# Optimization experiments

Measured on AMD Instinct MI355X. Metric: run time of the kernel, lower is better.

## Reference

```python
import jax, jax.numpy as jnp
import numpy as np

H = 256          # hidden_size
N_NODE = 50000   # item vocab
E_FULL = 500000  # full-graph edges
B = 1024         # sessions per batch
NODES_PER = 12   # session nodes per graph (contiguous, equal sections)
N = B * NODES_PER


def setup_inputs() -> dict:
    key = jax.random.key(0)
    ks = jax.random.split(key, 20)
    stdv = 1.0 / np.sqrt(H)
    u = lambda k, shape: jax.random.uniform(k, shape, jnp.float32, -stdv, stdv)
    return dict(
        x=jax.random.randint(ks[0], (N, 1), 1, N_NODE + 1, dtype=jnp.int32),  # 1-based item ids
        batch=jnp.repeat(jnp.arange(B, dtype=jnp.int32), NODES_PER),          # sorted graph ids
        edge_index=jax.random.randint(ks[1], (2, N), 0, N, dtype=jnp.int32),
        full_graph=jax.random.randint(ks[2], (2, E_FULL), 0, N_NODE, dtype=jnp.int32),
        emb=u(ks[3], (N_NODE, H)),
        ggnn_W=u(ks[4], (H, H)),
        gru_Wih=u(ks[5], (3 * H, H)),
        gru_Whh=u(ks[6], (3 * H, H)),
        gru_bih=u(ks[7], (3 * H,)),
        gru_bhh=u(ks[8], (3 * H,)),
        W1_w=u(ks[9], (H, H)), W1_b=u(ks[10], (H,)),
        W2_w=u(ks[11], (H, H)), W2_b=u(ks[12], (H,)),
        q_w=u(ks[13], (1, H)), q_b=u(ks[14], (1,)),
        W3_w=u(ks[15], (H, 2 * H)), W3_b=u(ks[16], (H,)),
    )


def _forward(x, batch, edge_index, full_graph, emb, ggnn_W, gru_Wih, gru_Whh,
             gru_bih, gru_bhh, W1_w, W1_b, W2_w, W2_b, q_w, q_b, W3_w, W3_b):
    # --- GatedGraphConv (num_layers=1) over the full item graph ---
    src, dst = full_graph[0], full_graph[1]
    m = emb @ ggnn_W                                      # [n_node, H]
    agg = jax.ops.segment_sum(m[src], dst, num_segments=N_NODE)  # sum aggregation
    # GRUCell(agg, emb)
    gi = agg @ gru_Wih.T + gru_bih                        # [n_node, 3H]
    gh = emb @ gru_Whh.T + gru_bhh
    i_r, i_z, i_n = jnp.split(gi, 3, axis=1)
    h_r, h_z, h_n = jnp.split(gh, 3, axis=1)
    r = jax.nn.sigmoid(i_r + h_r)
    z = jax.nn.sigmoid(i_z + h_z)
    n = jnp.tanh(i_n + r * h_n)
    hidden_all = (1.0 - z) * n + z * emb                  # [n_node, H]

    # gather session nodes (x is 1-based), relu
    h2 = jax.nn.relu(hidden_all[x[:, 0] - 1])             # [N, H]

    # --- Embedding2Score: segment attention readout ---
    sections = jax.ops.segment_sum(jnp.ones_like(batch), batch, num_segments=B)
    last_idx = jnp.cumsum(sections) - 1                   # last node of each session
    v_n = h2[last_idx]                                    # [B, H]
    v_n_rep = v_n[batch]                                  # [N, H]
    gate = jax.nn.sigmoid(v_n_rep @ W1_w.T + W1_b + h2 @ W2_w.T + W2_b)
    alpha = gate @ q_w.T + q_b                            # [N, 1]
    s_g = jax.ops.segment_sum(alpha * h2, batch, num_segments=B)  # [B, H]
    s_h = jnp.concatenate([v_n, s_g], axis=1) @ W3_w.T + W3_b     # [B, H]
    scores = s_h @ emb.T                                  # [B, n_node]
    return scores, h2


def reference(x, batch, edge_index, full_graph, emb, ggnn_W, gru_Wih, gru_Whh,
              gru_bih, gru_bhh, W1_w, W1_b, W2_w, W2_b, q_w, q_b, W3_w, W3_b):
    scores, h2 = _forward(x, batch, edge_index, full_graph, emb, ggnn_W,
                          gru_Wih, gru_Whh, gru_bih, gru_bhh,
                          W1_w, W1_b, W2_w, W2_b, q_w, q_b, W3_w, W3_b)
    return scores, h2, edge_index
```

## Files before the change

### kernel.cpp

```cpp
#include <hip/hip_runtime.h>
#include <hip/hip_bf16.h>
#include <stdint.h>

#define HDIM 256
#define NNODE 50000
#define EFULL 500000
#define BSESS 1024
#define NPER 12
#define NROWS 12288
#define CAP 96

typedef __attribute__((ext_vector_type(8))) short bf16x8;
typedef __attribute__((ext_vector_type(4))) float f32x4;
typedef __attribute__((ext_vector_type(4))) unsigned short u16x4;

__device__ __forceinline__ float bf2f(unsigned short v) {
  union { unsigned u; float f; } x; x.u = ((unsigned)v) << 16; return x.f;
}
__device__ __forceinline__ unsigned short f2bf(float f) {
  union { float f; unsigned u; } x; x.f = f;
  unsigned r = x.u + 0x7fff + ((x.u >> 16) & 1);
  return (unsigned short)(r >> 16);
}

__global__ void k_init_map(int* m, int* cnt) {
  int i = blockIdx.x * 256 + threadIdx.x;
  if (i < NNODE) m[i] = -1;
  if (i < NROWS) cnt[i] = 0;
}
__global__ void k_set_map(const int* __restrict__ x, int* __restrict__ m) {
  int i = blockIdx.x * 256 + threadIdx.x;
  if (i < NROWS) atomicMax(&m[x[i] - 1], i);
}

#define CV_EMB   12800000
#define CV_WT    65536
#define CV_WIH   196608
#define CV_WHH   196608
#define CV_W1    65536
#define CV_W2    65536
#define CV_W3    131072
#define CV_BIAS  2304
#define CV_TOTAL (CV_EMB + CV_WT + CV_WIH + CV_WHH + CV_W1 + CV_W2 + CV_W3 + CV_BIAS)
__global__ void k_conv(const float* __restrict__ emb, const float* __restrict__ gw,
                       const float* __restrict__ wih, const float* __restrict__ whh,
                       const float* __restrict__ w1, const float* __restrict__ w2,
                       const float* __restrict__ w3,
                       const float* __restrict__ bih, const float* __restrict__ bhh,
                       const float* __restrict__ w1b, const float* __restrict__ w2b,
                       const float* __restrict__ w3b,
                       unsigned short* __restrict__ embB, unsigned short* __restrict__ wtB,
                       unsigned short* __restrict__ wihB, unsigned short* __restrict__ whhB,
                       unsigned short* __restrict__ w1B, unsigned short* __restrict__ w2B,
                       unsigned short* __restrict__ w3B, unsigned short* __restrict__ biasB) {
  long idx = (long)blockIdx.x * 256 + threadIdx.x;
  if (idx < CV_EMB) { embB[idx] = f2bf(emb[idx]); return; }
  idx -= CV_EMB;
  if (idx < CV_WT) {
    int j = (int)(idx >> 8), k = (int)(idx & 255);
    wtB[idx] = f2bf(gw[k * 256 + j]); return;
  }
  idx -= CV_WT;
  if (idx < CV_WIH) { wihB[idx] = f2bf(wih[idx]); return; }
  idx -= CV_WIH;
  if (idx < CV_WHH) { whhB[idx] = f2bf(whh[idx]); return; }
  idx -= CV_WHH;
  if (idx < CV_W1)  { w1B[idx] = f2bf(w1[idx]); return; }
  idx -= CV_W1;
  if (idx < CV_W2)  { w2B[idx] = f2bf(w2[idx]); return; }
  idx -= CV_W2;
  if (idx < CV_W3)  { w3B[idx] = f2bf(w3[idx]); return; }
  idx -= CV_W3;
  if (idx < 768)        { biasB[idx] = f2bf(bih[idx]); return; }
  if (idx < 1536)       { biasB[idx] = f2bf(bhh[idx - 768]); return; }
  if (idx < 1792)       { biasB[idx] = f2bf(w1b[idx - 1536]); return; }
  if (idx < 2048)       { biasB[idx] = f2bf(w2b[idx - 1792]); return; }
  if (idx < CV_BIAS)    { biasB[idx] = f2bf(w3b[idx - 2048]); return; }
}

__global__ void k_bin(const int* __restrict__ fg, const int* __restrict__ map,
                      int* __restrict__ cnt, int* __restrict__ lists) {
  int e = blockIdx.x * 256 + threadIdx.x;
  if (e >= EFULL) return;
  int cid = map[fg[EFULL + e]];
  if (cid < 0) return;
  int pos = atomicAdd(&cnt[cid], 1);
  if (pos < CAP) lists[cid * CAP + pos] = fg[e];
}

__global__ __launch_bounds__(256) void k_aggsum(const int* __restrict__ cnt,
                                                const int* __restrict__ lists,
                                                const float* __restrict__ emb,
                                                unsigned short* __restrict__ Sb) {
  int i = blockIdx.x * 4 + (threadIdx.x >> 6);
  int lane = threadIdx.x & 63;
  int n = cnt[i];
  const int* lp = lists + (size_t)i * CAP;
  float sx = 0.f, sy = 0.f, sz = 0.f, sw = 0.f;
  int j = 0;
  for (; j + 4 <= n; j += 4) {
    int s0 = lp[j], s1 = lp[j + 1], s2 = lp[j + 2], s3 = lp[j + 3];
    float4 v0 = *(const float4*)(emb + (size_t)s0 * HDIM + lane * 4);
    float4 v1 = *(const float4*)(emb + (size_t)s1 * HDIM + lane * 4);
    float4 v2 = *(const float4*)(emb + (size_t)s2 * HDIM + lane * 4);
    float4 v3 = *(const float4*)(emb + (size_t)s3 * HDIM + lane * 4);
    sx += v0.x + v1.x + v2.x + v3.x;
    sy += v0.y + v1.y + v2.y + v3.y;
    sz += v0.z + v1.z + v2.z + v3.z;
    sw += v0.w + v1.w + v2.w + v3.w;
  }
  for (; j < n; j++) {
    int s0 = lp[j];
    float4 v0 = *(const float4*)(emb + (size_t)s0 * HDIM + lane * 4);
    sx += v0.x; sy += v0.y; sz += v0.z; sw += v0.w;
  }
  u16x4 o; o.x = f2bf(sx); o.y = f2bf(sy); o.z = f2bf(sz); o.w = f2bf(sw);
  *(u16x4*)(Sb + (size_t)i * HDIM + lane * 4) = o;
}

__global__ void k_gather(const int* __restrict__ x, const int* __restrict__ map,
                         const unsigned short* __restrict__ A2, const float* __restrict__ emb,
                         unsigned short* __restrict__ aggC, unsigned short* __restrict__ embC) {
  int i = blockIdx.x;
  int lane = threadIdx.x;
  int node = x[i] - 1;
  int cid = map[node];
  if (cid < 0) cid = 0;
  *(u16x4*)(aggC + (size_t)i * HDIM + lane * 4) = *(const u16x4*)(A2 + (size_t)cid * HDIM + lane * 4);
  float4 v = *(const float4*)(emb + (size_t)node * HDIM + lane * 4);
  u16x4 o; o.x = f2bf(v.x); o.y = f2bf(v.y); o.z = f2bf(v.z); o.w = f2bf(v.w);
  *(u16x4*)(embC + (size_t)i * HDIM + lane * 4) = o;
}
__global__ void k_gru(const unsigned short* __restrict__ gi, const unsigned short* __restrict__ gh,
                      const unsigned short* __restrict__ embC,
                      unsigned short* __restrict__ h2b, float* __restrict__ h2out) {
  int idx = blockIdx.x * 256 + threadIdx.x;
  size_t base = (size_t)(idx >> 8) * 768;
  int c = idx & 255;
  float ir = bf2f(gi[base + c]), iz = bf2f(gi[base + 256 + c]), inn = bf2f(gi[base + 512 + c]);
  float hr = bf2f(gh[base + c]), hz = bf2f(gh[base + 256 + c]), hn = bf2f(gh[base + 512 + c]);
  float r = 1.f / (1.f + expf(-(ir + hr)));
  float z = 1.f / (1.f + expf(-(iz + hz)));
  float n = tanhf(inn + r * hn);
  float h = fmaxf((1.f - z) * n + z * bf2f(embC[idx]), 0.f);
  h2b[idx] = f2bf(h);
  h2out[idx] = h;
}
__global__ void k_vn(const unsigned short* __restrict__ h2b, unsigned short* __restrict__ shin) {
  int idx = blockIdx.x * 256 + threadIdx.x;
  int b = idx >> 8, c = idx & 255;
  shin[(size_t)b * 512 + c] = h2b[((size_t)b * NPER + (NPER - 1)) * 256 + c];
}
__global__ void k_alpha(const unsigned short* __restrict__ t1, const unsigned short* __restrict__ t2,
                        const int* __restrict__ batch, const float* __restrict__ qw,
                        const float* __restrict__ qb, float* __restrict__ alpha) {
  int i = blockIdx.x, lane = threadIdx.x;
  int b = batch[i];
  u16x4 a = *(const u16x4*)(t1 + (size_t)b * HDIM + lane * 4);
  u16x4 c = *(const u16x4*)(t2 + (size_t)i * HDIM + lane * 4);
  float4 q = *(const float4*)(qw + lane * 4);
  float p = 0.f;
  p += q.x / (1.f + expf(-(bf2f(a.x) + bf2f(c.x))));
  p += q.y / (1.f + expf(-(bf2f(a.y) + bf2f(c.y))));
  p += q.z / (1.f + expf(-(bf2f(a.z) + bf2f(c.z))));
  p += q.w / (1.f + expf(-(bf2f(a.w) + bf2f(c.w))));
#pragma unroll
  for (int off = 32; off > 0; off >>= 1) p += __shfl_down(p, off);
  if (lane == 0) alpha[i] = p + qb[0];
}
__global__ void k_sg(const float* __restrict__ alpha, const unsigned short* __restrict__ h2b,
                     unsigned short* __restrict__ shin) {
  int b = blockIdx.x, c = threadIdx.x;
  float s = 0.f;
#pragma unroll
  for (int j = 0; j < NPER; j++)
    s += alpha[b * NPER + j] * bf2f(h2b[((size_t)b * NPER + j) * 256 + c]);
  shin[(size_t)b * 512 + 256 + c] = f2bf(s);
}
__global__ void k_edges(const int* __restrict__ e, float* __restrict__ out) {
  int i = blockIdx.x * 256 + threadIdx.x;
  if (i < 2 * NROWS) out[i] = (float)e[i];
}

template <bool OUT_BF16>
__global__ __launch_bounds__(256) void k_gemm_nt(
    const unsigned short* __restrict__ A, int lda,
    const unsigned short* __restrict__ Bm, int ldb,
    const unsigned short* __restrict__ bias,
    void* __restrict__ C, int ldc, int M, int N, int K) {
  __shared__ __align__(16) unsigned short As[128 * 32];
  __shared__ __align__(16) unsigned short Bs[128 * 32];
  const int tid = threadIdx.x;
  const int wid = tid >> 6, lane = tid & 63;
  const int quad = lane >> 4, l15 = lane & 15;
  const int m0 = blockIdx.x * 128, n0 = blockIdx.y * 128;
  const int wm = (wid & 1) * 64, wn = (wid >> 1) * 64;
  f32x4 acc[4][4] = {};
  const int lrow = tid >> 2;
  const int lcol = (tid & 3) * 8;
  const size_t ar0 = (size_t)min(m0 + lrow, M - 1) * lda + lcol;
  const size_t ar1 = (size_t)min(m0 + lrow + 64, M - 1) * lda + lcol;
  const size_t br0 = (size_t)min(n0 + lrow, N - 1) * ldb + lcol;
  const size_t br1 = (size_t)min(n0 + lrow + 64, N - 1) * ldb + lcol;
  const int ak = quad * 8;
  for (int k0 = 0; k0 < K; k0 += 32) {
    *(float4*)&As[(size_t)tid * 8]        = *(const float4*)&A[ar0 + k0];
    *(float4*)&As[2048 + (size_t)tid * 8] = *(const float4*)&A[ar1 + k0];
    *(float4*)&Bs[(size_t)tid * 8]        = *(const float4*)&Bm[br0 + k0];
    *(float4*)&Bs[2048 + (size_t)tid * 8] = *(const float4*)&Bm[br1 + k0];
    __syncthreads();
    bf16x8 af[4], bfv[4];
#pragma unroll
    for (int mi = 0; mi < 4; mi++) af[mi] = *(const bf16x8*)&As[(wm + mi * 16 + l15) * 32 + ak];
#pragma unroll
    for (int ni = 0; ni < 4; ni++) bfv[ni] = *(const bf16x8*)&Bs[(wn + ni * 16 + l15) * 32 + ak];
#pragma unroll
    for (int mi = 0; mi < 4; mi++)
#pragma unroll
      for (int ni = 0; ni < 4; ni++)
        acc[mi][ni] = __builtin_amdgcn_mfma_f32_16x16x32_bf16(af[mi], bfv[ni], acc[mi][ni], 0, 0, 0);
    __syncthreads();
  }
#pragma unroll
  for (int mi = 0; mi < 4; mi++) {
    const int gr0 = m0 + wm + mi * 16 + quad * 4;
#pragma unroll
    for (int ni = 0; ni < 4; ni++) {
      const int gc = n0 + wn + ni * 16 + l15;
      if (gc >= N) continue;
      const float bv = bias ? bf2f(bias[gc]) : 0.f;
#pragma unroll
      for (int r = 0; r < 4; r++) {
        const int gr = gr0 + r;
        if (gr < M) {
          const float v = acc[mi][ni][r] + bv;
          if (OUT_BF16) ((unsigned short*)C)[(size_t)gr * ldc + gc] = f2bf(v);
          else          ((float*)C)[(size_t)gr * ldc + gc] = v;
        }
      }
    }
  }
}

extern "C" void kernel_launch(void* const* d_in, const int* in_sizes, int n_in,
                              void* d_out, int out_size, void* d_ws, size_t ws_size,
                              hipStream_t stream) {
  const int* x     = (const int*)d_in[0];
  const int* batch = (const int*)d_in[1];
  const int* eidx  = (const int*)d_in[2];
  const int* fg    = (const int*)d_in[3];
  const float* emb   = (const float*)d_in[4];
  const float* ggnnW = (const float*)d_in[5];
  const float* Wih   = (const float*)d_in[6];
  const float* Whh   = (const float*)d_in[7];
  const float* bih   = (const float*)d_in[8];
  const float* bhh   = (const float*)d_in[9];
  const float* W1w   = (const float*)d_in[10];
  const float* W1b   = (const float*)d_in[11];
  const float* W2w   = (const float*)d_in[12];
  const float* W2b   = (const float*)d_in[13];
  const float* qw    = (const float*)d_in[14];
  const float* qb    = (const float*)d_in[15];
  const float* W3w   = (const float*)d_in[16];
  const float* W3b   = (const float*)d_in[17];

  char* w = (char*)d_ws;
  size_t off = 0;
  auto alloc = [&](size_t bytes) { char* p = w + off; off += (bytes + 511) & ~(size_t)511; return p; };
  unsigned short* giC  = (unsigned short*)alloc((size_t)NROWS * 768 * 2);
  unsigned short* Sb   = giC;
  int*            map  = (int*)alloc((size_t)NNODE * 4);
  int*            cnt  = (int*)alloc((size_t)NROWS * 4);
  int*            lists= (int*)alloc((size_t)NROWS * CAP * 4);
  unsigned short* A2   = (unsigned short*)alloc((size_t)NROWS * HDIM * 2);
  unsigned short* t2   = A2;
  unsigned short* aggC = (unsigned short*)alloc((size_t)NROWS * HDIM * 2);
  unsigned short* embC = (unsigned short*)alloc((size_t)NROWS * HDIM * 2);
  unsigned short* embB = (unsigned short*)alloc((size_t)NNODE * HDIM * 2);
  unsigned short* WTb  = (unsigned short*)alloc((size_t)CV_WT * 2);
  unsigned short* WihB = (unsigned short*)alloc((size_t)CV_WIH * 2);
  unsigned short* WhhB = (unsigned short*)alloc((size_t)CV_WHH * 2);
  unsigned short* W1wB = (unsigned short*)alloc((size_t)CV_W1 * 2);
  unsigned short* W2wB = (unsigned short*)alloc((size_t)CV_W2 * 2);
  unsigned short* W3wB = (unsigned short*)alloc((size_t)CV_W3 * 2);
  unsigned short* biasB= (unsigned short*)alloc((size_t)CV_BIAS * 2);
  unsigned short* ghC  = (unsigned short*)alloc((size_t)NROWS * 768 * 2);
  unsigned short* h2b  = (unsigned short*)alloc((size_t)NROWS * HDIM * 2);
  unsigned short* t1   = (unsigned short*)alloc((size_t)BSESS * HDIM * 2);
  float*          alpha = (float*)alloc((size_t)NROWS * 4);
  unsigned short* shin = (unsigned short*)alloc((size_t)BSESS * 512 * 2);
  unsigned short* shb  = (unsigned short*)alloc((size_t)BSESS * HDIM * 2);
  if (off > ws_size) return;

  float* out_scores = (float*)d_out;
  float* out_h2     = out_scores + (size_t)BSESS * NNODE;
  float* out_e      = out_h2 + (size_t)NROWS * HDIM;

  dim3 blk(256);
  k_init_map<<<(NNODE + 255) / 256, blk, 0, stream>>>(map, cnt);
  k_set_map <<<(NROWS + 255) / 256, blk, 0, stream>>>(x, map);
  k_conv    <<<(CV_TOTAL + 255) / 256, blk, 0, stream>>>(emb, ggnnW, Wih, Whh, W1w, W2w, W3w,
                bih, bhh, W1b, W2b, W3b, embB, WTb, WihB, WhhB, W1wB, W2wB, W3wB, biasB);
  k_bin     <<<(EFULL + 255) / 256, blk, 0, stream>>>(fg, map, cnt, lists);
  k_aggsum  <<<NROWS / 4, blk, 0, stream>>>(cnt, lists, emb, Sb);
  k_gemm_nt<true><<<dim3(96, 2), blk, 0, stream>>>(Sb, HDIM, WTb, HDIM, nullptr, A2, HDIM, NROWS, HDIM, HDIM);
  k_gather  <<<NROWS, 64, 0, stream>>>(x, map, A2, emb, aggC, embC);
  k_gemm_nt<true><<<dim3(96, 6), blk, 0, stream>>>(aggC, HDIM, WihB, HDIM, biasB, giC, 768, NROWS, 768, HDIM);
  k_gemm_nt<true><<<dim3(96, 6), blk, 0, stream>>>(embC, HDIM, WhhB, HDIM, biasB + 768, ghC, 768, NROWS, 768, HDIM);
  k_gru     <<<NROWS, blk, 0, stream>>>(giC, ghC, embC, h2b, out_h2);
  k_vn      <<<BSESS, blk, 0, stream>>>(h2b, shin);
  k_gemm_nt<true><<<dim3(8, 2), blk, 0, stream>>>(shin, 512, W1wB, HDIM, biasB + 1536, t1, HDIM, BSESS, HDIM, HDIM);
  k_gemm_nt<true><<<dim3(96, 2), blk, 0, stream>>>(h2b, HDIM, W2wB, HDIM, biasB + 1792, t2, HDIM, NROWS, HDIM, HDIM);
  k_alpha   <<<NROWS, 64, 0, stream>>>(t1, t2, batch, qw, qb, alpha);
  k_sg      <<<BSESS, blk, 0, stream>>>(alpha, h2b, shin);
  k_gemm_nt<true><<<dim3(8, 2), blk, 0, stream>>>(shin, 512, W3wB, 512, biasB + 2048, shb, HDIM, BSESS, HDIM, 512);
  k_gemm_nt<false><<<dim3(8, 391), blk, 0, stream>>>(shb, HDIM, embB, HDIM, nullptr, out_scores, NNODE, BSESS, NNODE, HDIM);
  k_edges   <<<(2 * NROWS + 255) / 256, blk, 0, stream>>>(eidx, out_e);
}
```

Baseline: 518.1 us.

## Fold GGNN weight into Wih and fuse GRU GEMMs into one concatenated GEMM

Precomputes Wih·Wᵀ once, so the per-row aggregation GEMM disappears and the aggregated sums feed the gate GEMM directly. The input- and hidden-side gate GEMMs are merged into one K=512 GEMM over a concatenated [agg | emb] activation. The r/z biases and pre-activations are summed inside that GEMM, which outputs 1024 columns instead of two 768-column outputs. k_vn is fused into the GRU kernel, and a new 256x128-tile, 512-thread MFMA GEMM is used for the fused gate GEMM and the large scores GEMM. Risks: the precomputed product is rounded to bf16 again, and the larger tiles may lower occupancy.

```diff
diff --git a/kernel.cpp b/kernel.cpp
--- a/kernel.cpp
+++ b/kernel.cpp
@@ -34,14 +34,14 @@
 }
 
 #define CV_EMB   12800000
-#define CV_WT    65536
+#define CV_GW    65536
 #define CV_WIH   196608
 #define CV_WHH   196608
 #define CV_W1    65536
 #define CV_W2    65536
 #define CV_W3    131072
 #define CV_BIAS  2304
-#define CV_TOTAL (CV_EMB + CV_WT + CV_WIH + CV_WHH + CV_W1 + CV_W2 + CV_W3 + CV_BIAS)
+#define CV_TOTAL (CV_EMB + CV_GW + CV_WIH + CV_WHH + CV_W1 + CV_W2 + CV_W3 + CV_BIAS)
 __global__ void k_conv(const float* __restrict__ emb, const float* __restrict__ gw,
                        const float* __restrict__ wih, const float* __restrict__ whh,
                        const float* __restrict__ w1, const float* __restrict__ w2,
@@ -49,18 +49,15 @@
                        const float* __restrict__ bih, const float* __restrict__ bhh,
                        const float* __restrict__ w1b, const float* __restrict__ w2b,
                        const float* __restrict__ w3b,
-                       unsigned short* __restrict__ embB, unsigned short* __restrict__ wtB,
+                       unsigned short* __restrict__ embB, unsigned short* __restrict__ gwB,
                        unsigned short* __restrict__ wihB, unsigned short* __restrict__ whhB,
                        unsigned short* __restrict__ w1B, unsigned short* __restrict__ w2B,
                        unsigned short* __restrict__ w3B, unsigned short* __restrict__ biasB) {
   long idx = (long)blockIdx.x * 256 + threadIdx.x;
   if (idx < CV_EMB) { embB[idx] = f2bf(emb[idx]); return; }
   idx -= CV_EMB;
-  if (idx < CV_WT) {
-    int j = (int)(idx >> 8), k = (int)(idx & 255);
-    wtB[idx] = f2bf(gw[k * 256 + j]); return;
-  }
-  idx -= CV_WT;
+  if (idx < CV_GW)  { gwB[idx] = f2bf(gw[idx]); return; }
+  idx -= CV_GW;
   if (idx < CV_WIH) { wihB[idx] = f2bf(wih[idx]); return; }
   idx -= CV_WIH;
   if (idx < CV_WHH) { whhB[idx] = f2bf(whh[idx]); return; }
@@ -118,39 +115,64 @@
   *(u16x4*)(Sb + (size_t)i * HDIM + lane * 4) = o;
 }
 
+__global__ void k_bbig(const unsigned short* __restrict__ Pt, const unsigned short* __restrict__ Whh,
+                       const float* __restrict__ bih, const float* __restrict__ bhh,
+                       unsigned short* __restrict__ Bbig, unsigned short* __restrict__ biasBig) {
+  int idx = blockIdx.x * 256 + threadIdx.x;
+  if (idx < 1024 * 512) {
+    int j = idx >> 9, c = idx & 511;
+    unsigned short v = 0;
+    if (c < 256) {
+      if (j < 768) v = Pt[j * 256 + c];
+    } else {
+      int cc = c - 256;
+      if (j < 512) v = Whh[j * 256 + cc];
+      else if (j >= 768) v = Whh[(j - 256) * 256 + cc];
+    }
+    Bbig[idx] = v;
+    return;
+  }
+  int jj = idx - 1024 * 512;
+  if (jj < 512)       biasBig[jj] = f2bf(bih[jj] + bhh[jj]);
+  else if (jj < 768)  biasBig[jj] = f2bf(bih[jj]);
+  else if (jj < 1024) biasBig[jj] = f2bf(bhh[jj - 256]);
+}
+
 __global__ void k_gather(const int* __restrict__ x, const int* __restrict__ map,
-                         const unsigned short* __restrict__ A2, const float* __restrict__ emb,
-                         unsigned short* __restrict__ aggC, unsigned short* __restrict__ embC) {
+                         const unsigned short* __restrict__ Sb, const float* __restrict__ emb,
+                         unsigned short* __restrict__ Acat) {
   int i = blockIdx.x;
   int lane = threadIdx.x;
   int node = x[i] - 1;
   int cid = map[node];
   if (cid < 0) cid = 0;
-  *(u16x4*)(aggC + (size_t)i * HDIM + lane * 4) = *(const u16x4*)(A2 + (size_t)cid * HDIM + lane * 4);
+  *(u16x4*)(Acat + (size_t)i * 512 + lane * 4) = *(const u16x4*)(Sb + (size_t)cid * HDIM + lane * 4);
   float4 v = *(const float4*)(emb + (size_t)node * HDIM + lane * 4);
   u16x4 o; o.x = f2bf(v.x); o.y = f2bf(v.y); o.z = f2bf(v.z); o.w = f2bf(v.w);
-  *(u16x4*)(embC + (size_t)i * HDIM + lane * 4) = o;
-}
-__global__ void k_gru(const unsigned short* __restrict__ gi, const unsigned short* __restrict__ gh,
-                      const unsigned short* __restrict__ embC,
-                      unsigned short* __restrict__ h2b, float* __restrict__ h2out) {
+  *(u16x4*)(Acat + (size_t)i * 512 + 256 + lane * 4) = o;
+}
+
+__global__ void k_gru(const unsigned short* __restrict__ gall, const unsigned short* __restrict__ Acat,
+                      unsigned short* __restrict__ h2b, float* __restrict__ h2out,
+                      unsigned short* __restrict__ shin) {
   int idx = blockIdx.x * 256 + threadIdx.x;
-  size_t base = (size_t)(idx >> 8) * 768;
-  int c = idx & 255;
-  float ir = bf2f(gi[base + c]), iz = bf2f(gi[base + 256 + c]), inn = bf2f(gi[base + 512 + c]);
-  float hr = bf2f(gh[base + c]), hz = bf2f(gh[base + 256 + c]), hn = bf2f(gh[base + 512 + c]);
-  float r = 1.f / (1.f + expf(-(ir + hr)));
-  float z = 1.f / (1.f + expf(-(iz + hz)));
+  int row = idx >> 8, c = idx & 255;
+  size_t base = (size_t)row * 1024;
+  float rs = bf2f(gall[base + c]);
+  float zs = bf2f(gall[base + 256 + c]);
+  float inn = bf2f(gall[base + 512 + c]);
+  float hn = bf2f(gall[base + 768 + c]);
+  float r = 1.f / (1.f + expf(-rs));
+  float z = 1.f / (1.f + expf(-zs));
   float n = tanhf(inn + r * hn);
-  float h = fmaxf((1.f - z) * n + z * bf2f(embC[idx]), 0.f);
-  h2b[idx] = f2bf(h);
+  float e = bf2f(Acat[(size_t)row * 512 + 256 + c]);
+  float h = fmaxf((1.f - z) * n + z * e, 0.f);
+  unsigned short hb = f2bf(h);
+  h2b[idx] = hb;
   h2out[idx] = h;
-}
-__global__ void k_vn(const unsigned short* __restrict__ h2b, unsigned short* __restrict__ shin) {
-  int idx = blockIdx.x * 256 + threadIdx.x;
-  int b = idx >> 8, c = idx & 255;
-  shin[(size_t)b * 512 + c] = h2b[((size_t)b * NPER + (NPER - 1)) * 256 + c];
-}
+  if (row % NPER == NPER - 1) shin[(size_t)(row / NPER) * 512 + c] = hb;
+}
+
 __global__ void k_alpha(const unsigned short* __restrict__ t1, const unsigned short* __restrict__ t2,
                         const int* __restrict__ batch, const float* __restrict__ qw,
                         const float* __restrict__ qb, float* __restrict__ alpha) {
@@ -242,6 +264,64 @@
   }
 }
 
+template <bool OUT_BF16>
+__global__ __launch_bounds__(512) void k_gemm_nt2(
+    const unsigned short* __restrict__ A, int lda,
+    const unsigned short* __restrict__ Bm, int ldb,
+    const unsigned short* __restrict__ bias,
+    void* __restrict__ C, int ldc, int M, int N, int K) {
+  __shared__ __align__(16) unsigned short As[256 * 32];
+  __shared__ __align__(16) unsigned short Bs[128 * 32];
+  const int tid = threadIdx.x;
+  const int wid = tid >> 6, lane = tid & 63;
+  const int quad = lane >> 4, l15 = lane & 15;
+  const int m0 = blockIdx.x * 256, n0 = blockIdx.y * 128;
+  const int wm = (wid & 3) * 64, wn = (wid >> 2) * 64;
+  f32x4 acc[4][4] = {};
+  const int lrow = tid >> 2;
+  const int lcol = (tid & 3) * 8;
+  const size_t ar0 = (size_t)min(m0 + lrow, M - 1) * lda + lcol;
+  const size_t ar1 = (size_t)min(m0 + lrow + 128, M - 1) * lda + lcol;
+  const size_t br0 = (size_t)min(n0 + lrow, N - 1) * ldb + lcol;
+  const int ak = quad * 8;
+  for (int k0 = 0; k0 < K; k0 += 32) {
+    *(float4*)&As[(size_t)lrow * 32 + lcol]         = *(const float4*)&A[ar0 + k0];
+    *(float4*)&As[(size_t)(lrow + 128) * 32 + lcol] = *(const float4*)&A[ar1 + k0];
+    *(float4*)&Bs[(size_t)lrow * 32 + lcol]         = *(const float4*)&Bm[br0 + k0];
+    __syncthreads();
+    bf16x8 af[4], bfv[4];
+#pragma unroll
+    for (int mi = 0; mi < 4; mi++) af[mi] = *(const bf16x8*)&As[(wm + mi * 16 + l15) * 32 + ak];
+#pragma unroll
+    for (int ni = 0; ni < 4; ni++) bfv[ni] = *(const bf16x8*)&Bs[(wn + ni * 16 + l15) * 32 + ak];
+#pragma unroll
+    for (int mi = 0; mi < 4; mi++)
+#pragma unroll
+      for (int ni = 0; ni < 4; ni++)
+        acc[mi][ni] = __builtin_amdgcn_mfma_f32_16x16x32_bf16(af[mi], bfv[ni], acc[mi][ni], 0, 0, 0);
+    __syncthreads();
+  }
+#pragma unroll
+  for (int mi = 0; mi < 4; mi++) {
+    const int gr0 = m0 + wm + mi * 16 + quad * 4;
+#pragma unroll
+    for (int ni = 0; ni < 4; ni++) {
+      const int gc = n0 + wn + ni * 16 + l15;
+      if (gc >= N) continue;
+      const float bv = bias ? bf2f(bias[gc]) : 0.f;
+#pragma unroll
+      for (int r = 0; r < 4; r++) {
+        const int gr = gr0 + r;
+        if (gr < M) {
+          const float v = acc[mi][ni][r] + bv;
+          if (OUT_BF16) ((unsigned short*)C)[(size_t)gr * ldc + gc] = f2bf(v);
+          else          ((float*)C)[(size_t)gr * ldc + gc] = v;
+        }
+      }
+    }
+  }
+}
+
 extern "C" void kernel_launch(void* const* d_in, const int* in_sizes, int n_in,
                               void* d_out, int out_size, void* d_ws, size_t ws_size,
                               hipStream_t stream) {
@@ -267,29 +347,29 @@
   char* w = (char*)d_ws;
   size_t off = 0;
   auto alloc = [&](size_t bytes) { char* p = w + off; off += (bytes + 511) & ~(size_t)511; return p; };
-  unsigned short* giC  = (unsigned short*)alloc((size_t)NROWS * 768 * 2);
-  unsigned short* Sb   = giC;
-  int*            map  = (int*)alloc((size_t)NNODE * 4);
-  int*            cnt  = (int*)alloc((size_t)NROWS * 4);
-  int*            lists= (int*)alloc((size_t)NROWS * CAP * 4);
-  unsigned short* A2   = (unsigned short*)alloc((size_t)NROWS * HDIM * 2);
-  unsigned short* t2   = A2;
-  unsigned short* aggC = (unsigned short*)alloc((size_t)NROWS * HDIM * 2);
-  unsigned short* embC = (unsigned short*)alloc((size_t)NROWS * HDIM * 2);
-  unsigned short* embB = (unsigned short*)alloc((size_t)NNODE * HDIM * 2);
-  unsigned short* WTb  = (unsigned short*)alloc((size_t)CV_WT * 2);
-  unsigned short* WihB = (unsigned short*)alloc((size_t)CV_WIH * 2);
-  unsigned short* WhhB = (unsigned short*)alloc((size_t)CV_WHH * 2);
-  unsigned short* W1wB = (unsigned short*)alloc((size_t)CV_W1 * 2);
-  unsigned short* W2wB = (unsigned short*)alloc((size_t)CV_W2 * 2);
-  unsigned short* W3wB = (unsigned short*)alloc((size_t)CV_W3 * 2);
-  unsigned short* biasB= (unsigned short*)alloc((size_t)CV_BIAS * 2);
-  unsigned short* ghC  = (unsigned short*)alloc((size_t)NROWS * 768 * 2);
-  unsigned short* h2b  = (unsigned short*)alloc((size_t)NROWS * HDIM * 2);
-  unsigned short* t1   = (unsigned short*)alloc((size_t)BSESS * HDIM * 2);
+  int*            map   = (int*)alloc((size_t)NNODE * 4);
+  int*            cnt   = (int*)alloc((size_t)NROWS * 4);
+  int*            lists = (int*)alloc((size_t)NROWS * CAP * 4);
+  unsigned short* Sb    = (unsigned short*)alloc((size_t)NROWS * HDIM * 2);
+  unsigned short* Acat  = (unsigned short*)alloc((size_t)NROWS * 512 * 2);
+  unsigned short* gallC = (unsigned short*)alloc((size_t)NROWS * 1024 * 2);
+  unsigned short* embB  = (unsigned short*)alloc((size_t)NNODE * HDIM * 2);
+  unsigned short* gwB   = (unsigned short*)alloc((size_t)CV_GW * 2);
+  unsigned short* WihB  = (unsigned short*)alloc((size_t)CV_WIH * 2);
+  unsigned short* WhhB  = (unsigned short*)alloc((size_t)CV_WHH * 2);
+  unsigned short* W1wB  = (unsigned short*)alloc((size_t)CV_W1 * 2);
+  unsigned short* W2wB  = (unsigned short*)alloc((size_t)CV_W2 * 2);
+  unsigned short* W3wB  = (unsigned short*)alloc((size_t)CV_W3 * 2);
+  unsigned short* biasB = (unsigned short*)alloc((size_t)CV_BIAS * 2);
+  unsigned short* Pt    = (unsigned short*)alloc((size_t)768 * 256 * 2);
+  unsigned short* Bbig  = (unsigned short*)alloc((size_t)1024 * 512 * 2);
+  unsigned short* biasBig = (unsigned short*)alloc((size_t)1024 * 2);
+  unsigned short* h2b   = (unsigned short*)alloc((size_t)NROWS * HDIM * 2);
+  unsigned short* t1    = (unsigned short*)alloc((size_t)BSESS * HDIM * 2);
+  unsigned short* t2    = (unsigned short*)alloc((size_t)NROWS * HDIM * 2);
   float*          alpha = (float*)alloc((size_t)NROWS * 4);
-  unsigned short* shin = (unsigned short*)alloc((size_t)BSESS * 512 * 2);
-  unsigned short* shb  = (unsigned short*)alloc((size_t)BSESS * HDIM * 2);
+  unsigned short* shin  = (unsigned short*)alloc((size_t)BSESS * 512 * 2);
+  unsigned short* shb   = (unsigned short*)alloc((size_t)BSESS * HDIM * 2);
   if (off > ws_size) return;
 
   float* out_scores = (float*)d_out;
@@ -300,20 +380,19 @@
   k_init_map<<<(NNODE + 255) / 256, blk, 0, stream>>>(map, cnt);
   k_set_map <<<(NROWS + 255) / 256, blk, 0, stream>>>(x, map);
   k_conv    <<<(CV_TOTAL + 255) / 256, blk, 0, stream>>>(emb, ggnnW, Wih, Whh, W1w, W2w, W3w,
-                bih, bhh, W1b, W2b, W3b, embB, WTb, WihB, WhhB, W1wB, W2wB, W3wB, biasB);
+                bih, bhh, W1b, W2b, W3b, embB, gwB, WihB, WhhB, W1wB, W2wB, W3wB, biasB);
   k_bin     <<<(EFULL + 255) / 256, blk, 0, stream>>>(fg, map, cnt, lists);
   k_aggsum  <<<NROWS / 4, blk, 0, stream>>>(cnt, lists, emb, Sb);
-  k_gemm_nt<true><<<dim3(96, 2), blk, 0, stream>>>(Sb, HDIM, WTb, HDIM, nullptr, A2, HDIM, NROWS, HDIM, HDIM);
-  k_gather  <<<NROWS, 64, 0, stream>>>(x, map, A2, emb, aggC, embC);
-  k_gemm_nt<true><<<dim3(96, 6), blk, 0, stream>>>(aggC, HDIM, WihB, HDIM, biasB, giC, 768, NROWS, 768, HDIM);
-  k_gemm_nt<true><<<dim3(96, 6), blk, 0, stream>>>(embC, HDIM, WhhB, HDIM, biasB + 768, ghC, 768, NROWS, 768, HDIM);
-  k_gru     <<<NROWS, blk, 0, stream>>>(giC, ghC, embC, h2b, out_h2);
-  k_vn      <<<BSESS, blk, 0, stream>>>(h2b, shin);
+  k_gemm_nt<true><<<dim3(6, 2), blk, 0, stream>>>(WihB, HDIM, gwB, HDIM, nullptr, Pt, HDIM, 768, HDIM, HDIM);
+  k_bbig    <<<(1024 * 512 + 1024 + 255) / 256, blk, 0, stream>>>(Pt, WhhB, bih, bhh, Bbig, biasBig);
+  k_gather  <<<NROWS, 64, 0, stream>>>(x, map, Sb, emb, Acat);
+  k_gemm_nt2<true><<<dim3(48, 8), dim3(512), 0, stream>>>(Acat, 512, Bbig, 512, biasBig, gallC, 1024, NROWS, 1024, 512);
+  k_gru     <<<NROWS, blk, 0, stream>>>(gallC, Acat, h2b, out_h2, shin);
   k_gemm_nt<true><<<dim3(8, 2), blk, 0, stream>>>(shin, 512, W1wB, HDIM, biasB + 1536, t1, HDIM, BSESS, HDIM, HDIM);
   k_gemm_nt<true><<<dim3(96, 2), blk, 0, stream>>>(h2b, HDIM, W2wB, HDIM, biasB + 1792, t2, HDIM, NROWS, HDIM, HDIM);
   k_alpha   <<<NROWS, 64, 0, stream>>>(t1, t2, batch, qw, qb, alpha);
   k_sg      <<<BSESS, blk, 0, stream>>>(alpha, h2b, shin);
   k_gemm_nt<true><<<dim3(8, 2), blk, 0, stream>>>(shin, 512, W3wB, 512, biasB + 2048, shb, HDIM, BSESS, HDIM, 512);
-  k_gemm_nt<false><<<dim3(8, 391), blk, 0, stream>>>(shb, HDIM, embB, HDIM, nullptr, out_scores, NNODE, BSESS, NNODE, HDIM);
+  k_gemm_nt2<false><<<dim3(4, 391), dim3(512), 0, stream>>>(shb, HDIM, embB, HDIM, nullptr, out_scores, NNODE, BSESS, NNODE, HDIM);
   k_edges   <<<(2 * NROWS + 255) / 256, blk, 0, stream>>>(eidx, out_e);
 }
```

Result: no change. 511.6 us (-1.2%).
